# Optimization experiments

Measured on AMD Instinct MI355X. Metric: run time of the kernel, lower is better.

## Reference

```python
import jax, jax.numpy as jnp
import numpy as np

B, T, DIN, E, HA, HB = 16, 128, 1024, 128, 128, 128


def setup_inputs() -> dict:
    key = jax.random.key(0)
    ks = jax.random.split(key, 12)
    u = lambda k, shape: jax.random.uniform(k, shape, jnp.float32, -0.1, 0.1)
    return {
        "x": jax.random.normal(ks[0], (B, T, DIN), jnp.float32),
        "W_emb": u(ks[1], (E, DIN)),
        "Wih_a": u(ks[2], (3 * HA, E)),
        "Whh_a": u(ks[3], (3 * HA, HA)),
        "bih_a": jnp.zeros((3 * HA,), jnp.float32),
        "bhh_a": jnp.zeros((3 * HA,), jnp.float32),
        "Wa": u(ks[4], (1, HA)),
        "ba": jnp.zeros((1,), jnp.float32),
        "Wih_b": u(ks[5], (3 * HB, E)),
        "Whh_b": u(ks[6], (3 * HB, HB)),
        "bih_b": jnp.zeros((3 * HB,), jnp.float32),
        "bhh_b": jnp.zeros((3 * HB,), jnp.float32),
        "Wb": u(ks[7], (E, HB)),
        "bb": jnp.zeros((E,), jnp.float32),
        "Wo": u(ks[8], (1, E)),
        "bo": jnp.zeros((1,), jnp.float32),
    }


def _gru_scan(x_seq, Wih, Whh, bih, bhh):
    # x_seq: (L, Ti, B, D) -> hidden states (L, Ti, B, H), PyTorch GRU gate math.
    H = Whh.shape[1]

    def step(h, x):
        gi = jnp.einsum('tbd,gd->tbg', x, Wih) + bih
        gh = jnp.einsum('tbh,gh->tbg', h, Whh) + bhh
        i_r, i_z, i_n = jnp.split(gi, 3, axis=-1)
        h_r, h_z, h_n = jnp.split(gh, 3, axis=-1)
        r = jax.nn.sigmoid(i_r + h_r)
        z = jax.nn.sigmoid(i_z + h_z)
        n = jnp.tanh(i_n + r * h_n)
        h2 = (1.0 - z) * n + z * h
        return h2, h2

    h0 = jnp.zeros(x_seq.shape[1:-1] + (H,), x_seq.dtype)
    _, hs = jax.lax.scan(step, h0, x_seq)
    return hs


def reference(x, W_emb, Wih_a, Whh_a, bih_a, bhh_a, Wa, ba,
              Wih_b, Whh_b, bih_b, bhh_b, Wb, bb, Wo, bo):
    emb = jnp.einsum('btd,ed->bte', x, W_emb)  # (B,T,E)
    Tn = emb.shape[1]
    i_idx = jnp.arange(Tn)
    k_idx = jnp.arange(Tn)
    # idx[i,k] = i-k (clipped): position j = i-k of the reversed prefix ending at i.
    idx = jnp.clip(i_idx[:, None] - k_idx[None, :], 0)
    # X_rev[k,i,b,:] = emb[b, i-k]  (reversed prefix inputs for every i at once)
    X_rev = jnp.transpose(emb[:, idx], (2, 1, 0, 3))  # (Tk,Ti,B,E)
    # Step k of the scan consumes temb[i-k] for every i simultaneously; outputs at
    # k<=i depend only on valid inputs, so padding (clipped k>i) never pollutes them.
    hs_a = _gru_scan(X_rev, Wih_a, Whh_a, bih_a, bhh_a) * 0.5  # (Tk,Ti,B,HA)
    hs_b = _gru_scan(X_rev, Wih_b, Whh_b, bih_b, bhh_b) * 0.5  # (Tk,Ti,B,HB)
    pre_alpha = jnp.einsum('kibh,oh->kib', hs_a, Wa) + ba[0]   # (Tk,Ti,B)
    valid = (k_idx[:, None] <= i_idx[None, :])[:, :, None]     # (Tk,Ti,1)
    pre_alpha = jnp.where(valid, pre_alpha, -1e30)
    alpha = jax.nn.softmax(pre_alpha, axis=0)                  # softmax over prefix positions
    beta = jnp.tanh(jnp.einsum('kibh,eh->kibe', hs_b, Wb) + bb)
    # context c[b,i,:] = sum_j alpha*beta*emb[j]; emb_rev == X_rev since use_time=False.
    c = jnp.einsum('kib,kibe->bie', alpha, beta * X_rev)       # (B,T,E)
    logits = jnp.einsum('bie,oe->bi', c, Wo) + bo[0]           # (B,T)
    return logits
```

## Files before the change

### kernel.cpp

```cpp
#include <hip/hip_runtime.h>
#include <hip/hip_bf16.h>

typedef unsigned int uint;
typedef unsigned short ushort;
typedef __attribute__((ext_vector_type(8))) short bf16x8;
typedef __attribute__((ext_vector_type(4))) float f32x4;

#define Tn 128
#define Bn 16
#define HH 128
#define G3 384
#define DIN 1024
#define PAD 136
#define SQP 132

#if __has_builtin(__builtin_amdgcn_cvt_pk_bf16_f32)
__device__ __forceinline__ uint pack2(float a, float b){
    auto v = __builtin_amdgcn_cvt_pk_bf16_f32(a, b);
    union { decltype(v) v2; uint u; } c; c.v2 = v;
    return c.u;
}
#else
__device__ __forceinline__ ushort f2bf_(float f){
    union{float f; uint u;} c; c.f = f;
    uint u = c.u + 0x7fffu + ((c.u >> 16) & 1u);
    return (ushort)(u >> 16);
}
__device__ __forceinline__ uint pack2(float a, float b){
    return ((uint)f2bf_(b) << 16) | (uint)f2bf_(a);
}
#endif
__device__ __forceinline__ ushort f2bf(float f){ return (ushort)(pack2(f, f) & 0xffffu); }

__device__ __forceinline__ float sigm(float x){ return 1.f/(1.f + __expf(-x)); }

__device__ __forceinline__ float rcpf(float x){ return __builtin_amdgcn_rcpf(x); }
__device__ __forceinline__ float tanh_rat(float x){
    x = fminf(5.f, fmaxf(-5.f, x));
    float t = x*x;
    float n = x*fmaf(t, fmaf(t, (t + 378.f), 17325.f), 135135.f);
    float d = fmaf(t, fmaf(t, fmaf(t, 28.f, 3150.f), 62370.f), 135135.f);
    return n * rcpf(d);
}
__device__ __forceinline__ float sig_num(float m, float t){
    return m*fmaf(t, fmaf(t, fmaf(t, 0.5f, 189.f), 8662.5f), 67567.5f);
}
__device__ __forceinline__ float sig_den(float t){
    return fmaf(t, fmaf(t, fmaf(t, 28.f, 3150.f), 62370.f), 135135.f);
}

__device__ __forceinline__ void bar_lds(){
    asm volatile("s_waitcnt lgkmcnt(0)\n\ts_barrier" ::: "memory");
}

__global__ __launch_bounds__(256) void k_cvt(const float* __restrict__ wemb,
                                             const float* __restrict__ wiha,
                                             const float* __restrict__ wihb,
                                             ushort* __restrict__ dst){
    int idx = (blockIdx.x*256 + threadIdx.x)*8;
    const float* s; int off;
    if (idx < 131072){ s = wemb; off = idx; }
    else if (idx < 180224){ s = wiha; off = idx - 131072; }
    else { s = wihb; off = idx - 180224; }
    float4 f0 = *(const float4*)(s + off);
    float4 f1 = *(const float4*)(s + off + 4);
    *(uint4*)(dst + idx) = (uint4){pack2(f0.x,f0.y),pack2(f0.z,f0.w),
                                   pack2(f1.x,f1.y),pack2(f1.z,f1.w)};
}

__global__ __launch_bounds__(512) void k_embgi(
    const float* __restrict__ x,      const ushort* __restrict__ WembB,
    const ushort* __restrict__ WihaB, const ushort* __restrict__ WihbB,
    const float* __restrict__ biha,   const float* __restrict__ bhha,
    const float* __restrict__ bihb,   const float* __restrict__ bhhb,
    const float* __restrict__ Wo,
    float* __restrict__ gia, float* __restrict__ gib, float* __restrict__ woE)
{
    __shared__ __align__(16) ushort LX[16*PAD];
    __shared__ __align__(16) ushort LW[128*PAD];
    __shared__ __align__(16) ushort LE[16*PAD];
    int tid = threadIdx.x;
    int lane = tid & 63, wave = tid >> 6;
    int quad = lane >> 4, n = lane & 15;
    int R0 = blockIdx.x * 16;
    int xr = tid >> 5, xc = (tid & 31) * 4;
    int wr2 = tid >> 2, wc2 = (tid & 3) * 32;

    f32x4 acc = {0.f,0.f,0.f,0.f};
    for (int kc = 0; kc < 8; ++kc){
        __syncthreads();
        {
            float4 v = *(const float4*)(x + (size_t)(R0 + xr)*DIN + kc*128 + xc);
            *(uint2*)&LX[xr*PAD + xc] = (uint2){pack2(v.x,v.y), pack2(v.z,v.w)};
            const uint4* sw = (const uint4*)(WembB + (size_t)wr2*DIN + kc*128 + wc2);
            uint4* dB = (uint4*)&LW[wr2*PAD + wc2];
            dB[0]=sw[0]; dB[1]=sw[1]; dB[2]=sw[2]; dB[3]=sw[3];
        }
        __syncthreads();
#pragma unroll
        for (int kb = 0; kb < 4; ++kb){
            bf16x8 a = *(const bf16x8*)&LX[n*PAD + kb*32 + quad*8];
            bf16x8 b = *(const bf16x8*)&LW[(wave*16 + n)*PAD + kb*32 + quad*8];
            acc = __builtin_amdgcn_mfma_f32_16x16x32_bf16(a, b, acc, 0,0,0);
        }
    }
    {
        int e = wave*16 + n;
        float wo = Wo[e];
#pragma unroll
        for (int l = 0; l < 4; ++l){
            int m = quad*4 + l;
            LE[m*PAD + e] = f2bf(acc[l]);
            int row = R0 + m, b_ = row >> 7, pos = row & 127;
            woE[((size_t)(pos*Bn + b_))*HH + e] = wo * acc[l];
        }
    }
    for (int nc = 0; nc < 6; ++nc){
        const ushort* Wsrc = (nc < 3) ? WihaB : WihbB;
        int gband = (nc < 3) ? nc : nc - 3;
        __syncthreads();
        {
            const uint4* sw = (const uint4*)(Wsrc + (size_t)(gband*128 + wr2)*HH + wc2);
            uint4* dB = (uint4*)&LW[wr2*PAD + wc2];
            dB[0]=sw[0]; dB[1]=sw[1]; dB[2]=sw[2]; dB[3]=sw[3];
        }
        __syncthreads();
        f32x4 gc = {0.f,0.f,0.f,0.f};
#pragma unroll
        for (int kb = 0; kb < 4; ++kb){
            bf16x8 a = *(const bf16x8*)&LE[n*PAD + kb*32 + quad*8];
            bf16x8 b = *(const bf16x8*)&LW[(wave*16 + n)*PAD + kb*32 + quad*8];
            gc = __builtin_amdgcn_mfma_f32_16x16x32_bf16(a, b, gc, 0,0,0);
        }
        int g = gband*128 + wave*16 + n;
        const float* bi = (nc < 3) ? biha : bihb;
        const float* bh = (nc < 3) ? bhha : bhhb;
        float bias = bi[g] + ((gband < 2) ? bh[g] : 0.f);
        float* dst = (nc < 3) ? gia : gib;
        int P = (3*wave + gband)*16 + n;
#pragma unroll
        for (int l = 0; l < 4; ++l){
            int row = R0 + quad*4 + l, b_ = row >> 7, pos = row & 127;
            dst[((size_t)(pos*Bn + b_))*G3 + P] = gc[l] + bias;
        }
    }
}

template<int GT>
__device__ __forceinline__ void gru_body(
    const float* __restrict__ Whh, const float* __restrict__ bhh,
    const float* __restrict__ Wsc, const float* __restrict__ bsc,
    const float* __restrict__ Gi,  const float* __restrict__ WoE,
    float* __restrict__ outW, int i)
{
    __shared__ __align__(16) ushort HF[2][2048];
    __shared__ __align__(16) ushort BFm[2][2048];
    __shared__ __align__(16) float SQ[16][SQP];
    int tid = threadIdx.x;
    int lane = tid & 63, wave = tid >> 6;
    int quad = lane >> 4, n = lane & 15;

    if (tid < 256) ((uint4*)HF[1])[tid] = (uint4){0,0,0,0};

    if (wave < 8){
        int u = wave, jb = u*16 + quad*4;
        bf16x8 afr[3][4];
#pragma unroll
        for (int g = 0; g < 3; ++g){
            const float* src = Whh + (size_t)(g*HH + u*16 + n)*HH;
#pragma unroll
            for (int kb = 0; kb < 4; ++kb){
                const float* p = src + kb*32 + quad*8;
                float4 a = *(const float4*)p, b2 = *(const float4*)(p+4);
                union { uint4 q; bf16x8 v; } cv;
                cv.q.x = pack2(a.x,a.y);   cv.q.y = pack2(a.z,a.w);
                cv.q.z = pack2(b2.x,b2.y); cv.q.w = pack2(b2.z,b2.w);
                afr[g][kb] = cv.v;
            }
        }
        float bh2[4];
#pragma unroll
        for (int l = 0; l < 4; ++l) bh2[l] = bhh[2*HH + jb + l];
        float h4[4] = {0.f,0.f,0.f,0.f};

        const float* gp = Gi + ((size_t)(i*Bn + n))*G3 + u*48 + quad*4;
        float4 pg0 = *(const float4*)(gp);
        float4 pg1 = *(const float4*)(gp + 16);
        float4 pg2 = *(const float4*)(gp + 32);
        bar_lds();

        for (int k = 0; k <= i; ++k){
            int pos = i - k;
            float4 g0 = pg0, g1 = pg1, g2 = pg2;
            int pnext = (pos > 0) ? pos - 1 : 0;
            const float* gp2 = Gi + ((size_t)(pnext*Bn + n))*G3 + u*48 + quad*4;
            pg0 = *(const float4*)(gp2);
            pg1 = *(const float4*)(gp2 + 16);
            pg2 = *(const float4*)(gp2 + 32);

            const ushort* HR = HF[(k+1)&1];
            f32x4 a0={0.f,0.f,0.f,0.f}, a1=a0, a2=a0;
#pragma unroll
            for (int kb = 0; kb < 4; ++kb){
                bf16x8 bfr = *(const bf16x8*)&HR[(64*kb + lane)*8];
                a0 = __builtin_amdgcn_mfma_f32_16x16x32_bf16(afr[0][kb], bfr, a0, 0,0,0);
                a1 = __builtin_amdgcn_mfma_f32_16x16x32_bf16(afr[1][kb], bfr, a1, 0,0,0);
                a2 = __builtin_amdgcn_mfma_f32_16x16x32_bf16(afr[2][kb], bfr, a2, 0,0,0);
            }
            float gi0[4]={g0.x,g0.y,g0.z,g0.w};
            float gi1[4]={g1.x,g1.y,g1.z,g1.w};
            float gi2[4]={g2.x,g2.y,g2.z,g2.w};
#pragma unroll
            for (int l = 0; l < 4; ++l){
                float mr = fminf(5.f, fmaxf(-5.f, 0.5f*(gi0[l] + a0[l])));
                float mz = fminf(5.f, fmaxf(-5.f, 0.5f*(gi1[l] + a1[l])));
                float tr = mr*mr, tz = mz*mz;
                float nr = sig_num(mr, tr), nz = sig_num(mz, tz);
                float dr = sig_den(tr),     dz = sig_den(tz);
                float rD = rcpf(dr*dz);
                float r = fmaf(nr*dz, rD, 0.5f);
                float z = fmaf(nz*dr, rD, 0.5f);
                float nn = tanh_rat(gi2[l] + r*(a2[l] + bh2[l]));
                h4[l] = nn + z*(h4[l] - nn);
            }
            *(uint2*)&HF[k&1][((jb>>3)*16 + n)*8 + (jb&4)] =
                (uint2){pack2(h4[0],h4[1]), pack2(h4[2],h4[3])};
            bar_lds();
        }
        if (GT){ bar_lds(); bar_lds(); } else { bar_lds(); }
    } else {
        int u2 = wave - 8, jb = u2*16 + quad*4;
        if (GT){
            bf16x8 afr3[4];
#pragma unroll
            for (int kb = 0; kb < 4; ++kb){
                const float* p = Wsc + (size_t)(u2*16 + n)*HH + kb*32 + quad*8;
                float4 a = *(const float4*)p, b2 = *(const float4*)(p+4);
                union { uint4 q; bf16x8 v; } cv;
                cv.q.x = pack2(0.5f*a.x, 0.5f*a.y);  cv.q.y = pack2(0.5f*a.z, 0.5f*a.w);
                cv.q.z = pack2(0.5f*b2.x,0.5f*b2.y); cv.q.w = pack2(0.5f*b2.z,0.5f*b2.w);
                afr3[kb] = cv.v;
            }
            bf16x8 onesf;
            {
                union { uint4 q; bf16x8 v; } c1;
                uint o = (n == 0) ? 0x3F803F80u : 0u;
                c1.q = (uint4){o,o,o,o};
                onesf = c1.v;
            }
            float bb4[4];
#pragma unroll
            for (int l = 0; l < 4; ++l) bb4[l] = bsc[jb + l];
            float4 pwo = *(const float4*)(WoE + ((size_t)(i*Bn + n))*HH + jb);
            bar_lds();

            for (int k = 0; k <= i; ++k){
                int pos = i - k;
                float4 wo = pwo;
                pwo = *(const float4*)(WoE + ((size_t)(pos*Bn + n))*HH + jb);

                const ushort* HR = HF[(k+1)&1];
                f32x4 a3 = {0.f,0.f,0.f,0.f};
#pragma unroll
                for (int kb = 0; kb < 4; ++kb){
                    bf16x8 bfr = *(const bf16x8*)&HR[(64*kb + lane)*8];
                    a3 = __builtin_amdgcn_mfma_f32_16x16x32_bf16(afr3[kb], bfr, a3, 0,0,0);
                }
                if (u2 == 0 && k >= 2){
                    const ushort* BR = BFm[(k+1)&1];
                    f32x4 qa = {0.f,0.f,0.f,0.f};
#pragma unroll
                    for (int kb = 0; kb < 4; ++kb){
                        bf16x8 bq = *(const bf16x8*)&BR[(64*kb + lane)*8];
                        qa = __builtin_amdgcn_mfma_f32_16x16x32_bf16(onesf, bq, qa, 0,0,0);
                    }
                    if (lane < 16) SQ[lane][k-2] = qa[0];
                }
                if (k >= 1){
                    float w0 = tanh_rat(a3[0]+bb4[0])*wo.x;
                    float w1 = tanh_rat(a3[1]+bb4[1])*wo.y;
                    float w2 = tanh_rat(a3[2]+bb4[2])*wo.z;
                    float w3 = tanh_rat(a3[3]+bb4[3])*wo.w;
                    *(uint2*)&BFm[k&1][((jb>>3)*16 + n)*8 + (jb&4)] =
                        (uint2){pack2(w0,w1), pack2(w2,w3)};
                }
                bar_lds();
            }
            {
                const ushort* HR = HF[i&1];
                f32x4 a3 = {0.f,0.f,0.f,0.f};
#pragma unroll
                for (int kb = 0; kb < 4; ++kb){
                    bf16x8 bfr = *(const bf16x8*)&HR[(64*kb + lane)*8];
                    a3 = __builtin_amdgcn_mfma_f32_16x16x32_bf16(afr3[kb], bfr, a3, 0,0,0);
                }
                float w0 = tanh_rat(a3[0]+bb4[0])*pwo.x;
                float w1 = tanh_rat(a3[1]+bb4[1])*pwo.y;
                float w2 = tanh_rat(a3[2]+bb4[2])*pwo.z;
                float w3 = tanh_rat(a3[3]+bb4[3])*pwo.w;
                *(uint2*)&BFm[(i+1)&1][((jb>>3)*16 + n)*8 + (jb&4)] =
                    (uint2){pack2(w0,w1), pack2(w2,w3)};
            }
            bar_lds();
            if (u2 == 0){
                if (i >= 1){
                    const ushort* BR = BFm[i&1];
                    f32x4 qa = {0.f,0.f,0.f,0.f};
#pragma unroll
                    for (int kb = 0; kb < 4; ++kb){
                        bf16x8 bq = *(const bf16x8*)&BR[(64*kb + lane)*8];
                        qa = __builtin_amdgcn_mfma_f32_16x16x32_bf16(onesf, bq, qa, 0,0,0);
                    }
                    if (lane < 16) SQ[lane][i-1] = qa[0];
                }
                {
                    const ushort* BR = BFm[(i+1)&1];
                    f32x4 qa = {0.f,0.f,0.f,0.f};
#pragma unroll
                    for (int kb = 0; kb < 4; ++kb){
                        bf16x8 bq = *(const bf16x8*)&BR[(64*kb + lane)*8];
                        qa = __builtin_amdgcn_mfma_f32_16x16x32_bf16(onesf, bq, qa, 0,0,0);
                    }
                    if (lane < 16) SQ[lane][i] = qa[0];
                }
            }
            bar_lds();
        } else {
            if (u2 == 0){
                bf16x8 afr3[4];
#pragma unroll
                for (int kb = 0; kb < 4; ++kb){
                    const float* p = Wsc + kb*32 + quad*8;
                    float4 a = *(const float4*)p, b2 = *(const float4*)(p+4);
                    union { uint4 q; bf16x8 v; } cv;
                    if (n == 0){
                        cv.q.x = pack2(0.5f*a.x, 0.5f*a.y);  cv.q.y = pack2(0.5f*a.z, 0.5f*a.w);
                        cv.q.z = pack2(0.5f*b2.x,0.5f*b2.y); cv.q.w = pack2(0.5f*b2.z,0.5f*b2.w);
                    } else cv.q = (uint4){0,0,0,0};
                    afr3[kb] = cv.v;
                }
                float bav = bsc[0];
                bar_lds();
                for (int k = 0; k <= i; ++k){
                    if (k >= 1){
                        const ushort* HR = HF[(k+1)&1];
                        f32x4 a3 = {0.f,0.f,0.f,0.f};
#pragma unroll
                        for (int kb = 0; kb < 4; ++kb){
                            bf16x8 bfr = *(const bf16x8*)&HR[(64*kb + lane)*8];
                            a3 = __builtin_amdgcn_mfma_f32_16x16x32_bf16(afr3[kb], bfr, a3, 0,0,0);
                        }
                        if (lane < 16) SQ[lane][k-1] = a3[0] + bav;
                    }
                    bar_lds();
                }
                {
                    const ushort* HR = HF[i&1];
                    f32x4 a3 = {0.f,0.f,0.f,0.f};
#pragma unroll
                    for (int kb = 0; kb < 4; ++kb){
                        bf16x8 bfr = *(const bf16x8*)&HR[(64*kb + lane)*8];
                        a3 = __builtin_amdgcn_mfma_f32_16x16x32_bf16(afr3[kb], bfr, a3, 0,0,0);
                    }
                    if (lane < 16) SQ[lane][i] = a3[0] + bav;
                }
                bar_lds();
            } else {
                bar_lds();
                for (int k = 0; k <= i; ++k) bar_lds();
                bar_lds();
            }
        }
    }
    if (tid < 512){
        int cn = tid >> 5, k4 = (tid & 31) * 4;
        *(float4*)&outW[((size_t)(cn*Tn + i))*Tn + k4] = *(const float4*)&SQ[cn][k4];
    }
}

__global__ __launch_bounds__(1024, 1) void k_gru(
    const float* __restrict__ WhhA, const float* __restrict__ bhhA,
    const float* __restrict__ Wa,   const float* __restrict__ ba,
    const float* __restrict__ WhhB, const float* __restrict__ bhhB,
    const float* __restrict__ Wb,   const float* __restrict__ bb,
    const float* __restrict__ GiA,  const float* __restrict__ GiB,
    const float* __restrict__ WoE,
    float* __restrict__ sW, float* __restrict__ qW)
{
    int i = Tn - 1 - (blockIdx.x >> 1);
    if ((blockIdx.x & 1) == 0) gru_body<0>(WhhA, bhhA, Wa, ba, GiA, nullptr, sW, i);
    else                       gru_body<1>(WhhB, bhhB, Wb, bb, GiB, WoE,    qW, i);
}

__global__ __launch_bounds__(256) void k_out(const float* __restrict__ sW,
                                             const float* __restrict__ qW,
                                             const float* __restrict__ bo,
                                             float* __restrict__ out){
    int tid = threadIdx.x, lane = tid & 63, w = tid >> 6;
    int r = blockIdx.x*4 + w;
    int i = r & (Tn-1);
    const float* s = sW + (size_t)r*Tn;
    const float* q = qW + (size_t)r*Tn;
    float s0 = (lane     <= i) ? s[lane]      : -1e30f;
    float s1 = (64+lane  <= i) ? s[64+lane]   : -1e30f;
    float m = fmaxf(s0, s1);
#pragma unroll
    for (int off = 32; off; off >>= 1) m = fmaxf(m, __shfl_xor(m, off));
    float e0 = __expf(s0 - m), e1 = __expf(s1 - m);
    float q0 = (lane    <= i) ? q[lane]    : 0.f;
    float q1 = (64+lane <= i) ? q[64+lane] : 0.f;
    float num = e0*q0 + e1*q1, den = e0 + e1;
#pragma unroll
    for (int off = 32; off; off >>= 1){
        num += __shfl_xor(num, off);
        den += __shfl_xor(den, off);
    }
    if (lane == 0) out[r] = num/den + bo[0];
}

extern "C" void kernel_launch(void* const* d_in, const int* in_sizes, int n_in,
                              void* d_out, int out_size, void* d_ws, size_t ws_size,
                              hipStream_t stream) {
    const float* x     = (const float*)d_in[0];
    const float* Wemb  = (const float*)d_in[1];
    const float* Wih_a = (const float*)d_in[2];
    const float* Whh_a = (const float*)d_in[3];
    const float* bih_a = (const float*)d_in[4];
    const float* bhh_a = (const float*)d_in[5];
    const float* Wa    = (const float*)d_in[6];
    const float* ba    = (const float*)d_in[7];
    const float* Wih_b = (const float*)d_in[8];
    const float* Whh_b = (const float*)d_in[9];
    const float* bih_b = (const float*)d_in[10];
    const float* bhh_b = (const float*)d_in[11];
    const float* Wb    = (const float*)d_in[12];
    const float* bb    = (const float*)d_in[13];
    const float* Wo    = (const float*)d_in[14];
    const float* bo    = (const float*)d_in[15];

    const int NR = Bn*Tn;
    float* giA = (float*)d_ws;
    float* giB = giA + (size_t)NR*G3;
    float* woE = giB + (size_t)NR*G3;
    float* sW  = woE + (size_t)NR*HH;
    float* qW  = sW + (size_t)NR*Tn;
    ushort* wcv = (ushort*)(qW + (size_t)NR*Tn);
    ushort* wembB = wcv;
    ushort* wihaB = wcv + 131072;
    ushort* wihbB = wcv + 180224;

    k_cvt<<<dim3(112), 256, 0, stream>>>(Wemb, Wih_a, Wih_b, wcv);
    k_embgi<<<dim3(128), 512, 0, stream>>>(x, wembB, wihaB, wihbB,
                                           bih_a, bhh_a, bih_b, bhh_b, Wo,
                                           giA, giB, woE);
    k_gru<<<dim3(256), 1024, 0, stream>>>(Whh_a, bhh_a, Wa, ba,
                                          Whh_b, bhh_b, Wb, bb,
                                          giA, giB, woE, sW, qW);
    k_out<<<dim3(NR/4), 256, 0, stream>>>(sW, qW, bo, (float*)d_out);
}
```

Baseline: 246.1 us.

## Double-buffer k_embgi staging, halve rows per block, fold sigmoid half-scale into weights

The embedding and input-gate kernel now double-buffers its LDS tiles, prefetching the next weight chunk from global memory while MFMAs run on the current one, with one barrier per chunk instead of two. Each block handles 8 rows padded to 16, so twice as many blocks launch, giving more parallelism at the cost of half-wasted MFMA rows. The 0.5 sigmoid pre-scale is folded into the r/z rows of Whh and into the precomputed input gates, removing a multiply per gate element in the serial GRU loop. Clamps now use fmed3, and the r/z clamp bound becomes ±4, which is equivalent to the old ±5 on half-scaled values only if the rational sigmoid approximation is accurate enough there.

```diff
diff --git a/kernel.cpp b/kernel.cpp
--- a/kernel.cpp
+++ b/kernel.cpp
@@ -32,11 +32,19 @@
 #endif
 __device__ __forceinline__ ushort f2bf(float f){ return (ushort)(pack2(f, f) & 0xffffu); }
 
-__device__ __forceinline__ float sigm(float x){ return 1.f/(1.f + __expf(-x)); }
+#if __has_builtin(__builtin_amdgcn_fmed3f)
+__device__ __forceinline__ float clampf(float x, float lo, float hi){
+    return __builtin_amdgcn_fmed3f(x, lo, hi);
+}
+#else
+__device__ __forceinline__ float clampf(float x, float lo, float hi){
+    return fminf(hi, fmaxf(lo, x));
+}
+#endif
 
 __device__ __forceinline__ float rcpf(float x){ return __builtin_amdgcn_rcpf(x); }
 __device__ __forceinline__ float tanh_rat(float x){
-    x = fminf(5.f, fmaxf(-5.f, x));
+    x = clampf(x, -5.f, 5.f);
     float t = x*x;
     float n = x*fmaf(t, fmaf(t, (t + 378.f), 17325.f), 135135.f);
     float d = fmaf(t, fmaf(t, fmaf(t, 28.f, 3150.f), 62370.f), 135135.f);
@@ -68,6 +76,15 @@
                                    pack2(f1.x,f1.y),pack2(f1.z,f1.w)};
 }
 
+__device__ __forceinline__ const uint4* stage_src(int c, const ushort* WembB,
+                                                  const ushort* WihaB,
+                                                  const ushort* WihbB,
+                                                  int wr2, int wc2){
+    if (c < 8)  return (const uint4*)(WembB + (size_t)wr2*DIN + c*128 + wc2);
+    if (c < 11) return (const uint4*)(WihaB + (size_t)((c-8)*128 + wr2)*HH + wc2);
+    return (const uint4*)(WihbB + (size_t)((c-11)*128 + wr2)*HH + wc2);
+}
+
 __global__ __launch_bounds__(512) void k_embgi(
     const float* __restrict__ x,      const ushort* __restrict__ WembB,
     const ushort* __restrict__ WihaB, const ushort* __restrict__ WihbB,
@@ -76,35 +93,51 @@
     const float* __restrict__ Wo,
     float* __restrict__ gia, float* __restrict__ gib, float* __restrict__ woE)
 {
-    __shared__ __align__(16) ushort LX[16*PAD];
-    __shared__ __align__(16) ushort LW[128*PAD];
+    __shared__ __align__(16) ushort LX[2][16*PAD];
+    __shared__ __align__(16) ushort LW[2][128*PAD];
     __shared__ __align__(16) ushort LE[16*PAD];
     int tid = threadIdx.x;
     int lane = tid & 63, wave = tid >> 6;
     int quad = lane >> 4, n = lane & 15;
-    int R0 = blockIdx.x * 16;
-    int xr = tid >> 5, xc = (tid & 31) * 4;
+    int R0 = blockIdx.x * 8;
+    int xr = tid >> 6, xc = (tid & 63) * 2;
     int wr2 = tid >> 2, wc2 = (tid & 3) * 32;
 
+    for (int z = tid; z < 544; z += 512){
+        ((uint*)&LX[0][8*PAD])[z] = 0;
+        ((uint*)&LX[1][8*PAD])[z] = 0;
+        ((uint*)&LE[8*PAD])[z]    = 0;
+    }
+    {
+        const uint4* s0 = stage_src(0, WembB, WihaB, WihbB, wr2, wc2);
+        uint4 a0=s0[0], a1=s0[1], a2=s0[2], a3=s0[3];
+        float2 v = *(const float2*)(x + (size_t)(R0 + xr)*DIN + xc);
+        uint4* d = (uint4*)&LW[0][wr2*PAD + wc2];
+        d[0]=a0; d[1]=a1; d[2]=a2; d[3]=a3;
+        *(uint*)&LX[0][xr*PAD + xc] = pack2(v.x, v.y);
+    }
+
     f32x4 acc = {0.f,0.f,0.f,0.f};
-    for (int kc = 0; kc < 8; ++kc){
-        __syncthreads();
+    for (int c = 0; c < 8; ++c){
+        bar_lds();
+        int cur = c & 1, nxt = cur ^ 1;
+        const uint4* sn = stage_src(c+1, WembB, WihaB, WihbB, wr2, wc2);
+        uint4 r0=sn[0], r1=sn[1], r2=sn[2], r3=sn[3];
+        float2 vx = {0.f,0.f};
+        if (c+1 < 8) vx = *(const float2*)(x + (size_t)(R0 + xr)*DIN + (c+1)*128 + xc);
+#pragma unroll
+        for (int kb = 0; kb < 4; ++kb){
+            bf16x8 a = *(const bf16x8*)&LX[cur][n*PAD + kb*32 + quad*8];
+            bf16x8 b = *(const bf16x8*)&LW[cur][(wave*16 + n)*PAD + kb*32 + quad*8];
+            acc = __builtin_amdgcn_mfma_f32_16x16x32_bf16(a, b, acc, 0,0,0);
+        }
         {
-            float4 v = *(const float4*)(x + (size_t)(R0 + xr)*DIN + kc*128 + xc);
-            *(uint2*)&LX[xr*PAD + xc] = (uint2){pack2(v.x,v.y), pack2(v.z,v.w)};
-            const uint4* sw = (const uint4*)(WembB + (size_t)wr2*DIN + kc*128 + wc2);
-            uint4* dB = (uint4*)&LW[wr2*PAD + wc2];
-            dB[0]=sw[0]; dB[1]=sw[1]; dB[2]=sw[2]; dB[3]=sw[3];
-        }
-        __syncthreads();
-#pragma unroll
-        for (int kb = 0; kb < 4; ++kb){
-            bf16x8 a = *(const bf16x8*)&LX[n*PAD + kb*32 + quad*8];
-            bf16x8 b = *(const bf16x8*)&LW[(wave*16 + n)*PAD + kb*32 + quad*8];
-            acc = __builtin_amdgcn_mfma_f32_16x16x32_bf16(a, b, acc, 0,0,0);
-        }
-    }
-    {
+            uint4* d = (uint4*)&LW[nxt][wr2*PAD + wc2];
+            d[0]=r0; d[1]=r1; d[2]=r2; d[3]=r3;
+            if (c+1 < 8) *(uint*)&LX[nxt][xr*PAD + xc] = pack2(vx.x, vx.y);
+        }
+    }
+    if (quad < 2){
         int e = wave*16 + n;
         float wo = Wo[e];
 #pragma unroll
@@ -115,33 +148,40 @@
             woE[((size_t)(pos*Bn + b_))*HH + e] = wo * acc[l];
         }
     }
-    for (int nc = 0; nc < 6; ++nc){
-        const ushort* Wsrc = (nc < 3) ? WihaB : WihbB;
-        int gband = (nc < 3) ? nc : nc - 3;
-        __syncthreads();
-        {
-            const uint4* sw = (const uint4*)(Wsrc + (size_t)(gband*128 + wr2)*HH + wc2);
-            uint4* dB = (uint4*)&LW[wr2*PAD + wc2];
-            dB[0]=sw[0]; dB[1]=sw[1]; dB[2]=sw[2]; dB[3]=sw[3];
-        }
-        __syncthreads();
+    for (int c = 8; c < 14; ++c){
+        bar_lds();
+        int cur = c & 1, nxt = cur ^ 1;
+        uint4 r0, r1, r2, r3;
+        if (c < 13){
+            const uint4* sn = stage_src(c+1, WembB, WihaB, WihbB, wr2, wc2);
+            r0=sn[0]; r1=sn[1]; r2=sn[2]; r3=sn[3];
+        }
         f32x4 gc = {0.f,0.f,0.f,0.f};
 #pragma unroll
         for (int kb = 0; kb < 4; ++kb){
             bf16x8 a = *(const bf16x8*)&LE[n*PAD + kb*32 + quad*8];
-            bf16x8 b = *(const bf16x8*)&LW[(wave*16 + n)*PAD + kb*32 + quad*8];
+            bf16x8 b = *(const bf16x8*)&LW[cur][(wave*16 + n)*PAD + kb*32 + quad*8];
             gc = __builtin_amdgcn_mfma_f32_16x16x32_bf16(a, b, gc, 0,0,0);
         }
+        int nc = c - 8;
+        int gband = (nc < 3) ? nc : nc - 3;
         int g = gband*128 + wave*16 + n;
         const float* bi = (nc < 3) ? biha : bihb;
         const float* bh = (nc < 3) ? bhha : bhhb;
         float bias = bi[g] + ((gband < 2) ? bh[g] : 0.f);
+        float scale = (gband < 2) ? 0.5f : 1.f;
         float* dst = (nc < 3) ? gia : gib;
         int P = (3*wave + gband)*16 + n;
-#pragma unroll
-        for (int l = 0; l < 4; ++l){
-            int row = R0 + quad*4 + l, b_ = row >> 7, pos = row & 127;
-            dst[((size_t)(pos*Bn + b_))*G3 + P] = gc[l] + bias;
+        if (quad < 2){
+#pragma unroll
+            for (int l = 0; l < 4; ++l){
+                int row = R0 + quad*4 + l, b_ = row >> 7, pos = row & 127;
+                dst[((size_t)(pos*Bn + b_))*G3 + P] = scale*(gc[l] + bias);
+            }
+        }
+        if (c < 13){
+            uint4* d = (uint4*)&LW[nxt][wr2*PAD + wc2];
+            d[0]=r0; d[1]=r1; d[2]=r2; d[3]=r3;
         }
     }
 }
@@ -168,13 +208,14 @@
 #pragma unroll
         for (int g = 0; g < 3; ++g){
             const float* src = Whh + (size_t)(g*HH + u*16 + n)*HH;
+            float s = (g < 2) ? 0.5f : 1.0f;
 #pragma unroll
             for (int kb = 0; kb < 4; ++kb){
                 const float* p = src + kb*32 + quad*8;
                 float4 a = *(const float4*)p, b2 = *(const float4*)(p+4);
                 union { uint4 q; bf16x8 v; } cv;
-                cv.q.x = pack2(a.x,a.y);   cv.q.y = pack2(a.z,a.w);
-                cv.q.z = pack2(b2.x,b2.y); cv.q.w = pack2(b2.z,b2.w);
+                cv.q.x = pack2(s*a.x, s*a.y);   cv.q.y = pack2(s*a.z, s*a.w);
+                cv.q.z = pack2(s*b2.x,s*b2.y); cv.q.w = pack2(s*b2.z,s*b2.w);
                 afr[g][kb] = cv.v;
             }
         }
@@ -212,8 +253,8 @@
             float gi2[4]={g2.x,g2.y,g2.z,g2.w};
 #pragma unroll
             for (int l = 0; l < 4; ++l){
-                float mr = fminf(5.f, fmaxf(-5.f, 0.5f*(gi0[l] + a0[l])));
-                float mz = fminf(5.f, fmaxf(-5.f, 0.5f*(gi1[l] + a1[l])));
+                float mr = clampf(gi0[l] + a0[l], -4.f, 4.f);
+                float mz = clampf(gi1[l] + a1[l], -4.f, 4.f);
                 float tr = mr*mr, tz = mz*mz;
                 float nr = sig_num(mr, tr), nz = sig_num(mz, tz);
                 float dr = sig_den(tr),     dz = sig_den(tz);
@@ -450,7 +491,7 @@
     ushort* wihbB = wcv + 180224;
 
     k_cvt<<<dim3(112), 256, 0, stream>>>(Wemb, Wih_a, Wih_b, wcv);
-    k_embgi<<<dim3(128), 512, 0, stream>>>(x, wembB, wihaB, wihbB,
+    k_embgi<<<dim3(256), 512, 0, stream>>>(x, wembB, wihaB, wihbB,
                                            bih_a, bhh_a, bih_b, bhh_b, Wo,
                                            giA, giB, woE);
     k_gru<<<dim3(256), 1024, 0, stream>>>(Whh_a, bhh_a, Wa, ba,
```

New measurement: 248.1 us. Within noise of the previous version (+0.8%).

## Fuse all stages into one cooperative kernel with grid-wide syncs

Applied to the files above, without the earlier changes.

Replaces the four separate launches (weight convert, embedding/input-gate GEMM, GRU scan, output softmax) with a single cooperative kernel of 256 blocks that runs each phase and separates them with grid syncs. The bf16 weight pre-conversion is folded into the embedding phase, and the GEMM is re-split so each block handles 8 rows. The 0.5 sigmoid scaling is folded into the precomputed input gates and the Whh r/z rows, and clamps use fmed3. This removes launch gaps and a kernel at the cost of grid-sync overhead and half-idle MFMA tiles in the embedding phase.

```diff
diff --git a/kernel.cpp b/kernel.cpp
--- a/kernel.cpp
+++ b/kernel.cpp
@@ -1,5 +1,8 @@
 #include <hip/hip_runtime.h>
 #include <hip/hip_bf16.h>
+#include <hip/hip_cooperative_groups.h>
+
+namespace cg = cooperative_groups;
 
 typedef unsigned int uint;
 typedef unsigned short ushort;
@@ -32,11 +35,19 @@
 #endif
 __device__ __forceinline__ ushort f2bf(float f){ return (ushort)(pack2(f, f) & 0xffffu); }
 
-__device__ __forceinline__ float sigm(float x){ return 1.f/(1.f + __expf(-x)); }
+#if __has_builtin(__builtin_amdgcn_fmed3f)
+__device__ __forceinline__ float clampf(float x, float lo, float hi){
+    return __builtin_amdgcn_fmed3f(x, lo, hi);
+}
+#else
+__device__ __forceinline__ float clampf(float x, float lo, float hi){
+    return fminf(hi, fmaxf(lo, x));
+}
+#endif
 
 __device__ __forceinline__ float rcpf(float x){ return __builtin_amdgcn_rcpf(x); }
 __device__ __forceinline__ float tanh_rat(float x){
-    x = fminf(5.f, fmaxf(-5.f, x));
+    x = clampf(x, -5.f, 5.f);
     float t = x*x;
     float n = x*fmaf(t, fmaf(t, (t + 378.f), 17325.f), 135135.f);
     float d = fmaf(t, fmaf(t, fmaf(t, 28.f, 3150.f), 62370.f), 135135.f);
@@ -53,58 +64,67 @@
     asm volatile("s_waitcnt lgkmcnt(0)\n\ts_barrier" ::: "memory");
 }
 
-__global__ __launch_bounds__(256) void k_cvt(const float* __restrict__ wemb,
-                                             const float* __restrict__ wiha,
-                                             const float* __restrict__ wihb,
-                                             ushort* __restrict__ dst){
-    int idx = (blockIdx.x*256 + threadIdx.x)*8;
-    const float* s; int off;
-    if (idx < 131072){ s = wemb; off = idx; }
-    else if (idx < 180224){ s = wiha; off = idx - 131072; }
-    else { s = wihb; off = idx - 180224; }
-    float4 f0 = *(const float4*)(s + off);
-    float4 f1 = *(const float4*)(s + off + 4);
-    *(uint4*)(dst + idx) = (uint4){pack2(f0.x,f0.y),pack2(f0.z,f0.w),
-                                   pack2(f1.x,f1.y),pack2(f1.z,f1.w)};
-}
-
-__global__ __launch_bounds__(512) void k_embgi(
-    const float* __restrict__ x,      const ushort* __restrict__ WembB,
-    const ushort* __restrict__ WihaB, const ushort* __restrict__ WihbB,
-    const float* __restrict__ biha,   const float* __restrict__ bhha,
-    const float* __restrict__ bihb,   const float* __restrict__ bhhb,
+struct SmemEmb {
+    ushort LX[16*PAD];
+    ushort LW[128*PAD];
+    ushort LE[16*PAD];
+};
+struct SmemGru {
+    ushort HF[2][2048];
+    ushort BFm[2][2048];
+    float  SQ[16][SQP];
+};
+union SmemU { SmemEmb e; SmemGru g; };
+
+__device__ void embgi_phase(SmemU& sm, int tid,
+    const float* __restrict__ x,    const float* __restrict__ Wemb,
+    const float* __restrict__ Wiha, const float* __restrict__ Wihb,
+    const float* __restrict__ biha, const float* __restrict__ bhha,
+    const float* __restrict__ bihb, const float* __restrict__ bhhb,
     const float* __restrict__ Wo,
-    float* __restrict__ gia, float* __restrict__ gib, float* __restrict__ woE)
+    float* __restrict__ gia, float* __restrict__ gib, float* __restrict__ woE,
+    int blk)
 {
-    __shared__ __align__(16) ushort LX[16*PAD];
-    __shared__ __align__(16) ushort LW[128*PAD];
-    __shared__ __align__(16) ushort LE[16*PAD];
-    int tid = threadIdx.x;
+    ushort* LX = sm.e.LX;
+    ushort* LW = sm.e.LW;
+    ushort* LE = sm.e.LE;
     int lane = tid & 63, wave = tid >> 6;
     int quad = lane >> 4, n = lane & 15;
-    int R0 = blockIdx.x * 16;
-    int xr = tid >> 5, xc = (tid & 31) * 4;
+    int R0 = blk * 8;
+    bool act = tid < 512;
+    int xr = tid >> 6, xc = (tid & 63) * 2;
     int wr2 = tid >> 2, wc2 = (tid & 3) * 32;
+
+    if (tid < 544){
+        ((uint*)&LX[8*PAD])[tid] = 0;
+        ((uint*)&LE[8*PAD])[tid] = 0;
+    }
 
     f32x4 acc = {0.f,0.f,0.f,0.f};
     for (int kc = 0; kc < 8; ++kc){
         __syncthreads();
-        {
-            float4 v = *(const float4*)(x + (size_t)(R0 + xr)*DIN + kc*128 + xc);
-            *(uint2*)&LX[xr*PAD + xc] = (uint2){pack2(v.x,v.y), pack2(v.z,v.w)};
-            const uint4* sw = (const uint4*)(WembB + (size_t)wr2*DIN + kc*128 + wc2);
+        if (act){
+            float2 v = *(const float2*)(x + (size_t)(R0 + xr)*DIN + kc*128 + xc);
+            *(uint*)&LX[xr*PAD + xc] = pack2(v.x, v.y);
+            const float4* sw = (const float4*)(Wemb + (size_t)wr2*DIN + kc*128 + wc2);
+            float4 g0=sw[0],g1=sw[1],g2=sw[2],g3=sw[3],g4=sw[4],g5=sw[5],g6=sw[6],g7=sw[7];
             uint4* dB = (uint4*)&LW[wr2*PAD + wc2];
-            dB[0]=sw[0]; dB[1]=sw[1]; dB[2]=sw[2]; dB[3]=sw[3];
+            dB[0] = (uint4){pack2(g0.x,g0.y),pack2(g0.z,g0.w),pack2(g1.x,g1.y),pack2(g1.z,g1.w)};
+            dB[1] = (uint4){pack2(g2.x,g2.y),pack2(g2.z,g2.w),pack2(g3.x,g3.y),pack2(g3.z,g3.w)};
+            dB[2] = (uint4){pack2(g4.x,g4.y),pack2(g4.z,g4.w),pack2(g5.x,g5.y),pack2(g5.z,g5.w)};
+            dB[3] = (uint4){pack2(g6.x,g6.y),pack2(g6.z,g6.w),pack2(g7.x,g7.y),pack2(g7.z,g7.w)};
         }
         __syncthreads();
-#pragma unroll
-        for (int kb = 0; kb < 4; ++kb){
-            bf16x8 a = *(const bf16x8*)&LX[n*PAD + kb*32 + quad*8];
-            bf16x8 b = *(const bf16x8*)&LW[(wave*16 + n)*PAD + kb*32 + quad*8];
-            acc = __builtin_amdgcn_mfma_f32_16x16x32_bf16(a, b, acc, 0,0,0);
-        }
-    }
-    {
+        if (act){
+#pragma unroll
+            for (int kb = 0; kb < 4; ++kb){
+                bf16x8 a = *(const bf16x8*)&LX[n*PAD + kb*32 + quad*8];
+                bf16x8 b = *(const bf16x8*)&LW[(wave*16 + n)*PAD + kb*32 + quad*8];
+                acc = __builtin_amdgcn_mfma_f32_16x16x32_bf16(a, b, acc, 0,0,0);
+            }
+        }
+    }
+    if (act && quad < 2){
         int e = wave*16 + n;
         float wo = Wo[e];
 #pragma unroll
@@ -116,46 +136,55 @@
         }
     }
     for (int nc = 0; nc < 6; ++nc){
-        const ushort* Wsrc = (nc < 3) ? WihaB : WihbB;
         int gband = (nc < 3) ? nc : nc - 3;
         __syncthreads();
-        {
-            const uint4* sw = (const uint4*)(Wsrc + (size_t)(gband*128 + wr2)*HH + wc2);
+        if (act){
+            const float* Wsrc = (nc < 3) ? Wiha : Wihb;
+            const float4* sw = (const float4*)(Wsrc + (size_t)(gband*128 + wr2)*HH + wc2);
+            float4 g0=sw[0],g1=sw[1],g2=sw[2],g3=sw[3],g4=sw[4],g5=sw[5],g6=sw[6],g7=sw[7];
             uint4* dB = (uint4*)&LW[wr2*PAD + wc2];
-            dB[0]=sw[0]; dB[1]=sw[1]; dB[2]=sw[2]; dB[3]=sw[3];
+            dB[0] = (uint4){pack2(g0.x,g0.y),pack2(g0.z,g0.w),pack2(g1.x,g1.y),pack2(g1.z,g1.w)};
+            dB[1] = (uint4){pack2(g2.x,g2.y),pack2(g2.z,g2.w),pack2(g3.x,g3.y),pack2(g3.z,g3.w)};
+            dB[2] = (uint4){pack2(g4.x,g4.y),pack2(g4.z,g4.w),pack2(g5.x,g5.y),pack2(g5.z,g5.w)};
+            dB[3] = (uint4){pack2(g6.x,g6.y),pack2(g6.z,g6.w),pack2(g7.x,g7.y),pack2(g7.z,g7.w)};
         }
         __syncthreads();
-        f32x4 gc = {0.f,0.f,0.f,0.f};
-#pragma unroll
-        for (int kb = 0; kb < 4; ++kb){
-            bf16x8 a = *(const bf16x8*)&LE[n*PAD + kb*32 + quad*8];
-            bf16x8 b = *(const bf16x8*)&LW[(wave*16 + n)*PAD + kb*32 + quad*8];
-            gc = __builtin_amdgcn_mfma_f32_16x16x32_bf16(a, b, gc, 0,0,0);
-        }
-        int g = gband*128 + wave*16 + n;
-        const float* bi = (nc < 3) ? biha : bihb;
-        const float* bh = (nc < 3) ? bhha : bhhb;
-        float bias = bi[g] + ((gband < 2) ? bh[g] : 0.f);
-        float* dst = (nc < 3) ? gia : gib;
-        int P = (3*wave + gband)*16 + n;
-#pragma unroll
-        for (int l = 0; l < 4; ++l){
-            int row = R0 + quad*4 + l, b_ = row >> 7, pos = row & 127;
-            dst[((size_t)(pos*Bn + b_))*G3 + P] = gc[l] + bias;
+        if (act){
+            f32x4 gc = {0.f,0.f,0.f,0.f};
+#pragma unroll
+            for (int kb = 0; kb < 4; ++kb){
+                bf16x8 a = *(const bf16x8*)&LE[n*PAD + kb*32 + quad*8];
+                bf16x8 b = *(const bf16x8*)&LW[(wave*16 + n)*PAD + kb*32 + quad*8];
+                gc = __builtin_amdgcn_mfma_f32_16x16x32_bf16(a, b, gc, 0,0,0);
+            }
+            int g = gband*128 + wave*16 + n;
+            const float* bi = (nc < 3) ? biha : bihb;
+            const float* bh = (nc < 3) ? bhha : bhhb;
+            float bias = bi[g] + ((gband < 2) ? bh[g] : 0.f);
+            float scale = (gband < 2) ? 0.5f : 1.f;
+            float* dst = (nc < 3) ? gia : gib;
+            int P = (3*wave + gband)*16 + n;
+            if (quad < 2){
+#pragma unroll
+                for (int l = 0; l < 4; ++l){
+                    int row = R0 + quad*4 + l, b_ = row >> 7, pos = row & 127;
+                    dst[((size_t)(pos*Bn + b_))*G3 + P] = scale*(gc[l] + bias);
+                }
+            }
         }
     }
 }
 
 template<int GT>
-__device__ __forceinline__ void gru_body(
+__device__ void gru_phase(SmemU& sm,
     const float* __restrict__ Whh, const float* __restrict__ bhh,
     const float* __restrict__ Wsc, const float* __restrict__ bsc,
     const float* __restrict__ Gi,  const float* __restrict__ WoE,
     float* __restrict__ outW, int i)
 {
-    __shared__ __align__(16) ushort HF[2][2048];
-    __shared__ __align__(16) ushort BFm[2][2048];
-    __shared__ __align__(16) float SQ[16][SQP];
+    auto& HF  = sm.g.HF;
+    auto& BFm = sm.g.BFm;
+    auto& SQ  = sm.g.SQ;
     int tid = threadIdx.x;
     int lane = tid & 63, wave = tid >> 6;
     int quad = lane >> 4, n = lane & 15;
@@ -168,13 +197,14 @@
 #pragma unroll
         for (int g = 0; g < 3; ++g){
             const float* src = Whh + (size_t)(g*HH + u*16 + n)*HH;
+            float s = (g < 2) ? 0.5f : 1.0f;
 #pragma unroll
             for (int kb = 0; kb < 4; ++kb){
                 const float* p = src + kb*32 + quad*8;
                 float4 a = *(const float4*)p, b2 = *(const float4*)(p+4);
                 union { uint4 q; bf16x8 v; } cv;
-                cv.q.x = pack2(a.x,a.y);   cv.q.y = pack2(a.z,a.w);
-                cv.q.z = pack2(b2.x,b2.y); cv.q.w = pack2(b2.z,b2.w);
+                cv.q.x = pack2(s*a.x, s*a.y);   cv.q.y = pack2(s*a.z, s*a.w);
+                cv.q.z = pack2(s*b2.x,s*b2.y); cv.q.w = pack2(s*b2.z,s*b2.w);
                 afr[g][kb] = cv.v;
             }
         }
@@ -212,8 +242,8 @@
             float gi2[4]={g2.x,g2.y,g2.z,g2.w};
 #pragma unroll
             for (int l = 0; l < 4; ++l){
-                float mr = fminf(5.f, fmaxf(-5.f, 0.5f*(gi0[l] + a0[l])));
-                float mz = fminf(5.f, fmaxf(-5.f, 0.5f*(gi1[l] + a1[l])));
+                float mr = clampf(gi0[l] + a0[l], -4.f, 4.f);
+                float mz = clampf(gi1[l] + a1[l], -4.f, 4.f);
                 float tr = mr*mr, tz = mz*mz;
                 float nr = sig_num(mr, tr), nz = sig_num(mz, tz);
                 float dr = sig_den(tr),     dz = sig_den(tz);
@@ -378,26 +408,12 @@
     }
 }
 
-__global__ __launch_bounds__(1024, 1) void k_gru(
-    const float* __restrict__ WhhA, const float* __restrict__ bhhA,
-    const float* __restrict__ Wa,   const float* __restrict__ ba,
-    const float* __restrict__ WhhB, const float* __restrict__ bhhB,
-    const float* __restrict__ Wb,   const float* __restrict__ bb,
-    const float* __restrict__ GiA,  const float* __restrict__ GiB,
-    const float* __restrict__ WoE,
-    float* __restrict__ sW, float* __restrict__ qW)
+__device__ void out_phase(const float* __restrict__ sW, const float* __restrict__ qW,
+                          const float* __restrict__ bo, float* __restrict__ out, int blk)
 {
-    int i = Tn - 1 - (blockIdx.x >> 1);
-    if ((blockIdx.x & 1) == 0) gru_body<0>(WhhA, bhhA, Wa, ba, GiA, nullptr, sW, i);
-    else                       gru_body<1>(WhhB, bhhB, Wb, bb, GiB, WoE,    qW, i);
-}
-
-__global__ __launch_bounds__(256) void k_out(const float* __restrict__ sW,
-                                             const float* __restrict__ qW,
-                                             const float* __restrict__ bo,
-                                             float* __restrict__ out){
-    int tid = threadIdx.x, lane = tid & 63, w = tid >> 6;
-    int r = blockIdx.x*4 + w;
+    int tid = threadIdx.x, lane = tid & 63, wave = tid >> 6;
+    if (wave >= 8) return;
+    int r = blk*8 + wave;
     int i = r & (Tn-1);
     const float* s = sW + (size_t)r*Tn;
     const float* q = qW + (size_t)r*Tn;
@@ -416,6 +432,34 @@
         den += __shfl_xor(den, off);
     }
     if (lane == 0) out[r] = num/den + bo[0];
+}
+
+__global__ __launch_bounds__(1024, 1) void k_fused(
+    const float* __restrict__ x,     const float* __restrict__ Wemb,
+    const float* __restrict__ Wih_a, const float* __restrict__ Whh_a,
+    const float* __restrict__ bih_a, const float* __restrict__ bhh_a,
+    const float* __restrict__ Wa,    const float* __restrict__ ba,
+    const float* __restrict__ Wih_b, const float* __restrict__ Whh_b,
+    const float* __restrict__ bih_b, const float* __restrict__ bhh_b,
+    const float* __restrict__ Wb,    const float* __restrict__ bb,
+    const float* __restrict__ Wo,    const float* __restrict__ bo,
+    float* __restrict__ giA, float* __restrict__ giB, float* __restrict__ woE,
+    float* __restrict__ sW,  float* __restrict__ qW,  float* __restrict__ out)
+{
+    __shared__ __align__(16) SmemU sm;
+    int tid = threadIdx.x;
+    int blk = blockIdx.x;
+
+    embgi_phase(sm, tid, x, Wemb, Wih_a, Wih_b, bih_a, bhh_a, bih_b, bhh_b, Wo,
+                giA, giB, woE, blk);
+    cg::this_grid().sync();
+
+    int i = Tn - 1 - (blk >> 1);
+    if ((blk & 1) == 0) gru_phase<0>(sm, Whh_a, bhh_a, Wa, ba, giA, nullptr, sW, i);
+    else                gru_phase<1>(sm, Whh_b, bhh_b, Wb, bb, giB, woE,    qW, i);
+    cg::this_grid().sync();
+
+    out_phase(sW, qW, bo, out, blk);
 }
 
 extern "C" void kernel_launch(void* const* d_in, const int* in_sizes, int n_in,
@@ -444,17 +488,15 @@
     float* woE = giB + (size_t)NR*G3;
     float* sW  = woE + (size_t)NR*HH;
     float* qW  = sW + (size_t)NR*Tn;
-    ushort* wcv = (ushort*)(qW + (size_t)NR*Tn);
-    ushort* wembB = wcv;
-    ushort* wihaB = wcv + 131072;
-    ushort* wihbB = wcv + 180224;
-
-    k_cvt<<<dim3(112), 256, 0, stream>>>(Wemb, Wih_a, Wih_b, wcv);
-    k_embgi<<<dim3(128), 512, 0, stream>>>(x, wembB, wihaB, wihbB,
-                                           bih_a, bhh_a, bih_b, bhh_b, Wo,
-                                           giA, giB, woE);
-    k_gru<<<dim3(256), 1024, 0, stream>>>(Whh_a, bhh_a, Wa, ba,
-                                          Whh_b, bhh_b, Wb, bb,
-                                          giA, giB, woE, sW, qW);
-    k_out<<<dim3(NR/4), 256, 0, stream>>>(sW, qW, bo, (float*)d_out);
-}
+    float* out = (float*)d_out;
+
+    void* args[] = {
+        (void*)&x, (void*)&Wemb, (void*)&Wih_a, (void*)&Whh_a,
+        (void*)&bih_a, (void*)&bhh_a, (void*)&Wa, (void*)&ba,
+        (void*)&Wih_b, (void*)&Whh_b, (void*)&bih_b, (void*)&bhh_b,
+        (void*)&Wb, (void*)&bb, (void*)&Wo, (void*)&bo,
+        (void*)&giA, (void*)&giB, (void*)&woE, (void*)&sW, (void*)&qW, (void*)&out
+    };
+    hipLaunchCooperativeKernel((const void*)k_fused, dim3(256), dim3(1024),
+                               args, 0, stream);
+}
```

Result: slower. 322.1 us (+30.9%).
